# Performance work log

Measured on AMD Instinct MI355X. Metric: run time of the kernel, lower is better.

## Reference

```python
import jax, jax.numpy as jnp
import numpy as np

B, S, H = 2, 4096, 2048
NH, NKV, HD = 16, 4, 128          # heads, kv heads, head_dim = H // NH
GS_RATIO = 0.25                    # hardcoded in MyAttention.forward
ROPE_BASE = 10000.0


def rotate_half(x):
    h = x.shape[-1] // 2
    return jnp.concatenate((-x[..., h:], x[..., :h]), axis=-1)


def setup_inputs() -> dict:
    key = jax.random.key(0)
    ks = jax.random.split(key, 5)
    g = int(S * GS_RATIO)
    hidden_states = jax.random.normal(ks[0], (B, S, H), jnp.float32)
    position_ids = jnp.tile(jnp.arange(S, dtype=jnp.int32)[None, :], (B, 1))
    # causal additive mask per group window (0 keep, -1e9 masked)
    i = jnp.arange(g)
    causal = i[None, :] <= i[:, None]
    attention_mask = jnp.broadcast_to(
        jnp.where(causal, 0.0, -1e9).astype(jnp.float32)[None, None], (B, 1, g, g)
    )
    sc = 0.02
    Wq = (jax.random.normal(ks[1], (H, NH * HD), jnp.float32) * sc)
    Wk = (jax.random.normal(ks[2], (H, NKV * HD), jnp.float32) * sc)
    Wv = (jax.random.normal(ks[3], (H, NKV * HD), jnp.float32) * sc)
    Wo = (jax.random.normal(ks[4], (NH * HD, H), jnp.float32) * sc)
    return {"hidden_states": hidden_states, "attention_mask": attention_mask,
            "position_ids": position_ids, "Wq": Wq, "Wk": Wk, "Wv": Wv, "Wo": Wo}


def reference(hidden_states, attention_mask, position_ids, Wq, Wk, Wv, Wo):
    B_, S_, H_ = hidden_states.shape
    g = int(S_ * GS_RATIO)
    ng = S_ // g
    n_rep = NH // NKV

    # QKV projections -> (B, heads, S, HD)
    q = (hidden_states @ Wq).reshape(B_, S_, NH, HD).transpose(0, 2, 1, 3)
    k = (hidden_states @ Wk).reshape(B_, S_, NKV, HD).transpose(0, 2, 1, 3)
    v = (hidden_states @ Wv).reshape(B_, S_, NKV, HD).transpose(0, 2, 1, 3)

    # RoPE
    inv_freq = 1.0 / (ROPE_BASE ** (jnp.arange(0, HD, 2, dtype=jnp.float32) / HD))
    t = jnp.arange(S_, dtype=jnp.float32)
    emb = jnp.concatenate([jnp.outer(t, inv_freq)] * 2, axis=-1)  # (S, HD)
    cos = jnp.cos(emb)[position_ids][:, None]  # (B,1,S,HD)
    sin = jnp.sin(emb)[position_ids][:, None]
    q = q * cos + rotate_half(q) * sin
    k = k * cos + rotate_half(k) * sin

    # GQA repeat_kv
    k = jnp.repeat(k, n_rep, axis=1)
    v = jnp.repeat(v, n_rep, axis=1)

    # S2-Attn shift: roll second half of heads by -g/2 along seq, then group
    def shift(x):
        x = jnp.concatenate([x[:, :NH // 2],
                             jnp.roll(x[:, NH // 2:], -g // 2, axis=2)], axis=1)
        return x.transpose(0, 2, 1, 3).reshape(B_ * ng, g, NH, HD).transpose(0, 2, 1, 3)

    q, k, v = shift(q), shift(k), shift(v)

    attn = jnp.einsum('bhqd,bhkd->bhqk', q, k) / np.float32(np.sqrt(HD))
    mask = jnp.tile(attention_mask, (ng, 1, 1, 1))  # (B*ng,1,g,g)
    attn = attn + mask
    attn = jax.nn.softmax(attn.astype(jnp.float32), axis=-1).astype(q.dtype)

    out = jnp.einsum('bhqk,bhkd->bhqd', attn, v)  # (B*ng, NH, g, HD)
    out = out.transpose(0, 2, 1, 3).reshape(B_, S_, NH, HD)
    # undo shift for second half of heads (+g/2 along seq)
    out = jnp.concatenate([out[:, :, :NH // 2],
                           jnp.roll(out[:, :, NH // 2:], g // 2, axis=1)], axis=2)
    out = out.reshape(B_, S_, NH * HD) @ Wo
    return out
```

## Files before the change

### kernel.cpp

```cpp
#include <hip/hip_runtime.h>
#include <math.h>

typedef unsigned short u16;
typedef short bf16x8 __attribute__((ext_vector_type(8)));
typedef float f32x4 __attribute__((ext_vector_type(4)));


__device__ __forceinline__ u16 f2bf(float x) {
  union { float f; unsigned u; } c; c.f = x;
  unsigned r = (c.u + 0x7FFFu + ((c.u >> 16) & 1u)) >> 16;
  return (u16)r;
}
__device__ __forceinline__ float bf2f(u16 x) {
  union { unsigned u; float f; } c; c.u = ((unsigned)x) << 16;
  return c.f;
}

#define GLD16(gp, lp)                                                   \
  __builtin_amdgcn_global_load_lds(                                     \
      (__attribute__((address_space(1))) void*)(gp),                    \
      (__attribute__((address_space(3))) void*)(lp), 16, 0, 0)

__global__ __launch_bounds__(256) void cast_bf16_vec(
    const float* __restrict__ X, u16* __restrict__ Y) {
  const size_t i = ((size_t)blockIdx.x * 256 + threadIdx.x) * 4;
  float4 v = *(const float4*)(X + i);
  ushort4 o;
  o.x = f2bf(v.x); o.y = f2bf(v.y); o.z = f2bf(v.z); o.w = f2bf(v.w);
  *(ushort4*)(Y + i) = o;
}

__global__ __launch_bounds__(256) void wt_cast(
    const float* __restrict__ W, u16* __restrict__ Wt, int K, int N) {
  const int bk = blockIdx.y * 64;
  const int bn = blockIdx.x * 64;
  __shared__ float T[64 * 65];
  const int tid = threadIdx.x;
  #pragma unroll
  for (int u = 0; u < 16; ++u) {
    int idx = tid + u * 256;
    int kl = idx >> 6, nl = idx & 63;
    T[kl * 65 + nl] = W[(size_t)(bk + kl) * N + bn + nl];
  }
  __syncthreads();
  #pragma unroll
  for (int u = 0; u < 16; ++u) {
    int idx = tid + u * 256;
    int nl = idx >> 6, kl = idx & 63;
    Wt[(size_t)(bn + nl) * K + bk + kl] = f2bf(T[kl * 65 + nl]);
  }
}

__global__ __launch_bounds__(256) void gemm_bf16(
    const u16* __restrict__ A, const u16* __restrict__ Bt,
    float* __restrict__ Cf, u16* __restrict__ Cb, int M, int N, int K) {
  __shared__ u16 As[128 * 32];
  __shared__ u16 Bs[128 * 32];

  const int tid = threadIdx.x;
  const int bm = blockIdx.y * 128;
  const int bn = blockIdx.x * 128;
  const int w = tid >> 6, lane = tid & 63;
  const int col = lane & 15, quad = lane >> 4;
  const int mblk = (w & 1) * 64, nblk = (w >> 1) * 64;

  const int srow = tid >> 2;
  const int sseg = (tid & 3) * 8;

  const u16* ag0 = A + (size_t)(bm + srow) * K + sseg;
  const u16* ag1 = A + (size_t)(bm + 64 + srow) * K + sseg;
  const u16* bg0 = Bt + (size_t)(bn + srow) * K + sseg;
  const u16* bg1 = Bt + (size_t)(bn + 64 + srow) * K + sseg;
  u16* al = &As[srow * 32 + sseg];
  u16* bl = &Bs[srow * 32 + sseg];

  f32x4 acc[4][4];
  #pragma unroll
  for (int i = 0; i < 4; ++i)
    #pragma unroll
    for (int j = 0; j < 4; ++j) acc[i][j] = (f32x4)(0.0f);

  for (int k0 = 0; k0 < K; k0 += 32) {
    __syncthreads();
    GLD16(ag0 + k0, al);
    GLD16(ag1 + k0, al + 64 * 32);
    GLD16(bg0 + k0, bl);
    GLD16(bg1 + k0, bl + 64 * 32);
    __syncthreads();

    bf16x8 af[4], bfr[4];
    #pragma unroll
    for (int i = 0; i < 4; ++i)
      af[i] = *(const bf16x8*)&As[(mblk + 16 * i + col) * 32 + quad * 8];
    #pragma unroll
    for (int j = 0; j < 4; ++j)
      bfr[j] = *(const bf16x8*)&Bs[(nblk + 16 * j + col) * 32 + quad * 8];
    #pragma unroll
    for (int i = 0; i < 4; ++i)
      #pragma unroll
      for (int j = 0; j < 4; ++j)
        acc[i][j] = __builtin_amdgcn_mfma_f32_16x16x32_bf16(af[i], bfr[j], acc[i][j], 0, 0, 0);
  }

  #pragma unroll
  for (int i = 0; i < 4; ++i) {
    const int row0 = bm + mblk + 16 * i + quad * 4;
    #pragma unroll
    for (int j = 0; j < 4; ++j) {
      const int cc = bn + nblk + 16 * j + col;
      #pragma unroll
      for (int r = 0; r < 4; ++r) {
        if (Cb) Cb[(size_t)(row0 + r) * N + cc] = f2bf(acc[i][j][r]);
        else    Cf[(size_t)(row0 + r) * N + cc] = acc[i][j][r];
      }
    }
  }
}

__global__ __launch_bounds__(256) void rope_qkv(
    u16* __restrict__ QKV, const int* __restrict__ pos) {
  const unsigned idx = blockIdx.x * 256 + threadIdx.x;
  const int d = idx & 63;
  const unsigned rest = idx >> 6;
  const int hh = rest % 20;
  const unsigned bs = rest / 20;

  const int colbase = (hh < 16) ? hh * 128 : 2048 + (hh - 16) * 128;
  u16* p = QKV + (size_t)bs * 3072 + colbase + d;
  const float x0 = bf2f(p[0]);
  const float x1 = bf2f(p[64]);
  const float t = (float)pos[bs];
  const float inv_freq = __expf((float)d * -0.14391156509676332f);
  float s, c;
  __sincosf(t * inv_freq, &s, &c);
  const float sc = (hh < 16) ? 0.08838834764831845f : 1.0f;
  p[0]  = f2bf((x0 * c - x1 * s) * sc);
  p[64] = f2bf((x1 * c + x0 * s) * sc);
}

__global__ __launch_bounds__(256) void v_transpose(
    const u16* __restrict__ QKV, u16* __restrict__ Vt) {
  const int bid = blockIdx.x;
  const int st = bid & 63;
  const int kvh = (bid >> 6) & 3;
  const int b = bid >> 8;
  __shared__ u16 T[64 * 136];
  const int tid = threadIdx.x;
  #pragma unroll
  for (int u = 0; u < 4; ++u) {
    int idx = tid + u * 256;
    int sl = idx >> 4, ch = idx & 15;
    *(uint4*)&T[sl * 136 + ch * 8] =
        *(const uint4*)(QKV + ((size_t)(b * 4096 + st * 64 + sl)) * 3072 + 2560 + kvh * 128 + ch * 8);
  }
  __syncthreads();
  #pragma unroll
  for (int u = 0; u < 32; ++u) {
    int idx = tid + u * 256;
    int d = idx >> 6, sl = idx & 63;
    Vt[((size_t)((b * 4 + kvh) * 128 + d)) * 4096 + st * 64 + sl] = T[sl * 136 + d];
  }
}

__global__ __launch_bounds__(256) void attn_mfma(
    const u16* __restrict__ QKV, const u16* __restrict__ Vt,
    u16* __restrict__ Ob) {
  __shared__ u16 Ks[64 * 136];
  __shared__ u16 Vs[128 * 72];
  __shared__ u16 Ps[4][16 * 72];

  const int bid = blockIdx.x;
  const int qt = 15 - (bid & 15);
  const int h  = (bid >> 4) & 15;
  const int gi = (bid >> 8) & 3;
  const int b  = bid >> 10;

  const int tid = threadIdx.x;
  const int w = tid >> 6, lane = tid & 63;
  const int col = lane & 15, quad = lane >> 4;

  const int shift = (h >= 8) ? 512 : 0;
  const int base_s = gi * 1024;
  const int kvh = h >> 2;

  const int sq0 = (base_s + qt * 64 + shift) & 4095;
  {
    const u16* qsrc = QKV + ((size_t)(b * 4096 + sq0)) * 3072 + h * 128;
    #pragma unroll
    for (int u = 0; u < 4; ++u) {
      int idx = tid + u * 256;
      int row = idx >> 4, ch = idx & 15;
      *(uint4*)&Ks[row * 136 + ch * 8] =
          *(const uint4*)(qsrc + (size_t)row * 3072 + ch * 8);
    }
  }
  __syncthreads();
  bf16x8 aq[4];
  #pragma unroll
  for (int kk = 0; kk < 4; ++kk)
    aq[kk] = *(const bf16x8*)&Ks[(w * 16 + col) * 136 + kk * 32 + quad * 8];

  f32x4 o[8];
  #pragma unroll
  for (int jd = 0; jd < 8; ++jd) o[jd] = (f32x4)(0.0f);
  float lp[4] = {0.0f, 0.0f, 0.0f, 0.0f};

  u16* Pw = &Ps[w][0];
  const int qrow_l = w * 16 + quad * 4;

  for (int kt = 0; kt <= qt; ++kt) {
    const int sk0 = (base_s + kt * 64 + shift) & 4095;
    __syncthreads();
    {
      const u16* ksrc = QKV + ((size_t)(b * 4096 + sk0)) * 3072 + 2048 + kvh * 128;
      #pragma unroll
      for (int u = 0; u < 4; ++u) {
        int idx = tid + u * 256;
        int row = idx >> 4, ch = idx & 15;
        *(uint4*)&Ks[row * 136 + ch * 8] =
            *(const uint4*)(ksrc + (size_t)row * 3072 + ch * 8);
      }
      const u16* vsrc = Vt + ((size_t)((b * 4 + kvh) * 128)) * 4096 + sk0;
      #pragma unroll
      for (int u = 0; u < 4; ++u) {
        int idx = tid + u * 256;
        int d = idx >> 3, ch = idx & 7;
        *(uint4*)&Vs[d * 72 + ch * 8] =
            *(const uint4*)(vsrc + (size_t)d * 4096 + ch * 8);
      }
    }
    __syncthreads();

    f32x4 sc[4];
    #pragma unroll
    for (int j = 0; j < 4; ++j) sc[j] = (f32x4)(0.0f);
    #pragma unroll
    for (int kk = 0; kk < 4; ++kk) {
      #pragma unroll
      for (int j = 0; j < 4; ++j) {
        bf16x8 bk = *(const bf16x8*)&Ks[(16 * j + col) * 136 + kk * 32 + quad * 8];
        sc[j] = __builtin_amdgcn_mfma_f32_16x16x32_bf16(aq[kk], bk, sc[j], 0, 0, 0);
      }
    }

    #pragma unroll
    for (int j = 0; j < 4; ++j) {
      #pragma unroll
      for (int r = 0; r < 4; ++r) {
        float p = __expf(sc[j][r]);
        if (kt == qt && (16 * j + col) > (qrow_l + r)) p = 0.0f;
        lp[r] += p;
        Pw[(quad * 4 + r) * 72 + 16 * j + col] = f2bf(p);
      }
    }

    #pragma unroll
    for (int ks = 0; ks < 2; ++ks) {
      bf16x8 ap = *(const bf16x8*)&Pw[col * 72 + ks * 32 + quad * 8];
      #pragma unroll
      for (int jd = 0; jd < 8; ++jd) {
        bf16x8 bv = *(const bf16x8*)&Vs[(16 * jd + col) * 72 + ks * 32 + quad * 8];
        o[jd] = __builtin_amdgcn_mfma_f32_16x16x32_bf16(ap, bv, o[jd], 0, 0, 0);
      }
    }
  }

  #pragma unroll
  for (int r = 0; r < 4; ++r) {
    lp[r] += __shfl_xor(lp[r], 1, 64);
    lp[r] += __shfl_xor(lp[r], 2, 64);
    lp[r] += __shfl_xor(lp[r], 4, 64);
    lp[r] += __shfl_xor(lp[r], 8, 64);
  }

  #pragma unroll
  for (int r = 0; r < 4; ++r) {
    const int qg = qt * 64 + w * 16 + quad * 4 + r;
    const int sq = (base_s + qg + shift) & 4095;
    u16* dst = Ob + ((size_t)(b * 4096 + sq)) * 2048 + h * 128;
    const float inv = 1.0f / lp[r];
    #pragma unroll
    for (int jd = 0; jd < 8; ++jd)
      dst[16 * jd + col] = f2bf(o[jd][r] * inv);
  }
}

extern "C" void kernel_launch(void* const* d_in, const int* in_sizes, int n_in,
                              void* d_out, int out_size, void* d_ws, size_t ws_size,
                              hipStream_t stream) {
  const float* hs = (const float*)d_in[0];
  const int*   pos = (const int*)d_in[2];
  const float* Wq = (const float*)d_in[3];
  const float* Wk = (const float*)d_in[4];
  const float* Wv = (const float*)d_in[5];
  const float* Wo = (const float*)d_in[6];

  char* ws = (char*)d_ws;
  u16* hsb   = (u16*)ws; ws += (size_t)8192 * 2048 * 2;
  u16* Wqkvt = (u16*)ws; ws += (size_t)3072 * 2048 * 2;
  u16* Wot   = (u16*)ws; ws += (size_t)2048 * 2048 * 2;
  u16* QKVb  = (u16*)ws; ws += (size_t)8192 * 3072 * 2;
  u16* Vtt   = (u16*)ws; ws += (size_t)2 * 4 * 128 * 4096 * 2;
  u16* Obh   = (u16*)ws; ws += (size_t)8192 * 2048 * 2;

  dim3 blk(256);

  cast_bf16_vec<<<16384, blk, 0, stream>>>(hs, hsb);
  wt_cast<<<dim3(32, 32), blk, 0, stream>>>(Wq, Wqkvt, 2048, 2048);
  wt_cast<<<dim3(8, 32),  blk, 0, stream>>>(Wk, Wqkvt + (size_t)2048 * 2048, 2048, 512);
  wt_cast<<<dim3(8, 32),  blk, 0, stream>>>(Wv, Wqkvt + (size_t)2560 * 2048, 2048, 512);
  wt_cast<<<dim3(32, 32), blk, 0, stream>>>(Wo, Wot, 2048, 2048);

  gemm_bf16<<<dim3(24, 64), blk, 0, stream>>>(hsb, Wqkvt, nullptr, QKVb, 8192, 3072, 2048);

  rope_qkv<<<40960, blk, 0, stream>>>(QKVb, pos);

  v_transpose<<<512, blk, 0, stream>>>(QKVb, Vtt);

  attn_mfma<<<2048, blk, 0, stream>>>(QKVb, Vtt, Obh);

  gemm_bf16<<<dim3(16, 64), blk, 0, stream>>>(Obh, Wot, (float*)d_out, nullptr, 8192, 2048, 2048);
}
```

Measured before the change: 584.5 us.

## Replace GEMM with 256x256-tile, 512-thread, multi-buffered pipelined kernel

Both projection GEMMs move to a new kernel with 256x256 output tiles and 8 waves. It uses a 4-deep LDS ring with prefetch two k-steps ahead via global_load_lds, plus an XOR swizzle against LDS bank conflicts. Workgroup IDs are remapped so consecutive tiles land on the same XCD for L2 reuse, and s_setprio and split MFMA phases interleave loads with compute. The aim is to raise data reuse and hide memory latency, at the cost of a larger LDS footprint (64KB) and fewer, larger workgroups.

```diff
diff --git a/kernel.cpp b/kernel.cpp
--- a/kernel.cpp
+++ b/kernel.cpp
@@ -51,63 +51,120 @@
   }
 }
 
-__global__ __launch_bounds__(256) void gemm_bf16(
+__global__ __launch_bounds__(512) void gemm_bf16_256(
     const u16* __restrict__ A, const u16* __restrict__ Bt,
     float* __restrict__ Cf, u16* __restrict__ Cb, int M, int N, int K) {
-  __shared__ u16 As[128 * 32];
-  __shared__ u16 Bs[128 * 32];
+  __shared__ u16 As[4][256 * 32];
+  __shared__ u16 Bs[4][256 * 32];
 
   const int tid = threadIdx.x;
-  const int bm = blockIdx.y * 128;
-  const int bn = blockIdx.x * 128;
+
+  const int gridN = N >> 8;
+  const int nwg = gridDim.x * gridDim.y;
+  const int orig = blockIdx.y * gridDim.x + blockIdx.x;
+  const int q8 = nwg >> 3, r8 = nwg & 7;
+  const int xcd = orig & 7, lid = orig >> 3;
+  const int wgid = (xcd < r8 ? xcd * (q8 + 1) : r8 * (q8 + 1) + (xcd - r8) * q8) + lid;
+  const int bm = (wgid / gridN) << 8;
+  const int bn = (wgid % gridN) << 8;
+
   const int w = tid >> 6, lane = tid & 63;
   const int col = lane & 15, quad = lane >> 4;
-  const int mblk = (w & 1) * 64, nblk = (w >> 1) * 64;
+  const int wm = w >> 2, wn = w & 3;
+  const int sw = (col >> 1) & 3;
 
   const int srow = tid >> 2;
-  const int sseg = (tid & 3) * 8;
-
-  const u16* ag0 = A + (size_t)(bm + srow) * K + sseg;
-  const u16* ag1 = A + (size_t)(bm + 64 + srow) * K + sseg;
-  const u16* bg0 = Bt + (size_t)(bn + srow) * K + sseg;
-  const u16* bg1 = Bt + (size_t)(bn + 64 + srow) * K + sseg;
-  u16* al = &As[srow * 32 + sseg];
-  u16* bl = &Bs[srow * 32 + sseg];
-
-  f32x4 acc[4][4];
-  #pragma unroll
-  for (int i = 0; i < 4; ++i)
+  const int scp  = tid & 3;
+  const int sc   = scp ^ ((srow >> 1) & 3);
+
+  const u16* Ag = A  + (size_t)bm * K;
+  const u16* Bg = Bt + (size_t)bn * K;
+  const u16* aS0 = Ag + (size_t)srow * K + sc * 8;
+  const u16* aS1 = Ag + (size_t)(srow + 128) * K + sc * 8;
+  const u16* bS0 = Bg + (size_t)srow * K + sc * 8;
+  const u16* bS1 = Bg + (size_t)(srow + 128) * K + sc * 8;
+  const int ldst0 = srow * 32 + scp * 8;
+  const int ldst1 = (srow + 128) * 32 + scp * 8;
+
+#define STAGE_A(t, buf) { GLD16(aS0 + (size_t)(t) * 32, &As[buf][ldst0]); \
+                          GLD16(aS1 + (size_t)(t) * 32, &As[buf][ldst1]); }
+#define STAGE_B(t, buf) { GLD16(bS0 + (size_t)(t) * 32, &Bs[buf][ldst0]); \
+                          GLD16(bS1 + (size_t)(t) * 32, &Bs[buf][ldst1]); }
+
+  f32x4 acc[8][4];
+  #pragma unroll
+  for (int i = 0; i < 8; ++i)
     #pragma unroll
     for (int j = 0; j < 4; ++j) acc[i][j] = (f32x4)(0.0f);
 
-  for (int k0 = 0; k0 < K; k0 += 32) {
-    __syncthreads();
-    GLD16(ag0 + k0, al);
-    GLD16(ag1 + k0, al + 64 * 32);
-    GLD16(bg0 + k0, bl);
-    GLD16(bg1 + k0, bl + 64 * 32);
-    __syncthreads();
+  const int NT = K >> 5;
+
+  STAGE_A(0, 0); STAGE_B(0, 0);
+  if (NT > 1) {
+    STAGE_A(1, 1); STAGE_B(1, 1);
+    asm volatile("s_waitcnt vmcnt(4)" ::: "memory");
+  } else {
+    asm volatile("s_waitcnt vmcnt(0)" ::: "memory");
+  }
+  __builtin_amdgcn_s_barrier();
+  asm volatile("" ::: "memory");
+
+  const int aoff = (wm * 128 + col) * 32 + (quad ^ sw) * 8;
+  const int boff = (wn * 64  + col) * 32 + (quad ^ sw) * 8;
+
+  for (int t = 0; t < NT; ++t) {
+    const int cur = t & 3;
+    const bool pf = (t + 2 < NT);
+    const int pbuf = (t + 2) & 3;
 
     bf16x8 af[4], bfr[4];
     #pragma unroll
     for (int i = 0; i < 4; ++i)
-      af[i] = *(const bf16x8*)&As[(mblk + 16 * i + col) * 32 + quad * 8];
+      af[i] = *(const bf16x8*)&As[cur][aoff + (16 * i) * 32];
     #pragma unroll
     for (int j = 0; j < 4; ++j)
-      bfr[j] = *(const bf16x8*)&Bs[(nblk + 16 * j + col) * 32 + quad * 8];
+      bfr[j] = *(const bf16x8*)&Bs[cur][boff + (16 * j) * 32];
+    if (pf) STAGE_A(t + 2, pbuf);
+    __builtin_amdgcn_s_barrier();
+    asm volatile("s_waitcnt lgkmcnt(0)");
+    __builtin_amdgcn_s_setprio(1);
     #pragma unroll
     for (int i = 0; i < 4; ++i)
       #pragma unroll
       for (int j = 0; j < 4; ++j)
         acc[i][j] = __builtin_amdgcn_mfma_f32_16x16x32_bf16(af[i], bfr[j], acc[i][j], 0, 0, 0);
-  }
-
-  #pragma unroll
-  for (int i = 0; i < 4; ++i) {
-    const int row0 = bm + mblk + 16 * i + quad * 4;
+    __builtin_amdgcn_s_setprio(0);
+    __builtin_amdgcn_s_barrier();
+
+    bf16x8 af2[4];
+    #pragma unroll
+    for (int i = 0; i < 4; ++i)
+      af2[i] = *(const bf16x8*)&As[cur][aoff + ((64 + 16 * i)) * 32];
+    if (pf) STAGE_B(t + 2, pbuf);
+    __builtin_amdgcn_s_barrier();
+    asm volatile("s_waitcnt lgkmcnt(0)");
+    __builtin_amdgcn_s_setprio(1);
+    #pragma unroll
+    for (int i = 0; i < 4; ++i)
+      #pragma unroll
+      for (int j = 0; j < 4; ++j)
+        acc[4 + i][j] = __builtin_amdgcn_mfma_f32_16x16x32_bf16(af2[i], bfr[j], acc[4 + i][j], 0, 0, 0);
+    __builtin_amdgcn_s_setprio(0);
+
+    if (pf) asm volatile("s_waitcnt vmcnt(4)" ::: "memory");
+    else    asm volatile("s_waitcnt vmcnt(0)" ::: "memory");
+    __builtin_amdgcn_s_barrier();
+    asm volatile("" ::: "memory");
+  }
+
+  const int crow0 = bm + wm * 128 + quad * 4;
+  const int ccol0 = bn + wn * 64 + col;
+  #pragma unroll
+  for (int i = 0; i < 8; ++i) {
+    const int row0 = crow0 + 16 * i;
     #pragma unroll
     for (int j = 0; j < 4; ++j) {
-      const int cc = bn + nblk + 16 * j + col;
+      const int cc = ccol0 + 16 * j;
       #pragma unroll
       for (int r = 0; r < 4; ++r) {
         if (Cb) Cb[(size_t)(row0 + r) * N + cc] = f2bf(acc[i][j][r]);
@@ -115,6 +172,8 @@
       }
     }
   }
+#undef STAGE_A
+#undef STAGE_B
 }
 
 __global__ __launch_bounds__(256) void rope_qkv(
@@ -311,7 +370,7 @@
   wt_cast<<<dim3(8, 32),  blk, 0, stream>>>(Wv, Wqkvt + (size_t)2560 * 2048, 2048, 512);
   wt_cast<<<dim3(32, 32), blk, 0, stream>>>(Wo, Wot, 2048, 2048);
 
-  gemm_bf16<<<dim3(24, 64), blk, 0, stream>>>(hsb, Wqkvt, nullptr, QKVb, 8192, 3072, 2048);
+  gemm_bf16_256<<<dim3(12, 32), dim3(512), 0, stream>>>(hsb, Wqkvt, nullptr, QKVb, 8192, 3072, 2048);
 
   rope_qkv<<<40960, blk, 0, stream>>>(QKVb, pos);
 
@@ -319,5 +378,5 @@
 
   attn_mfma<<<2048, blk, 0, stream>>>(QKVb, Vtt, Obh);
 
-  gemm_bf16<<<dim3(16, 64), blk, 0, stream>>>(Obh, Wot, (float*)d_out, nullptr, 8192, 2048, 2048);
-}
+  gemm_bf16_256<<<dim3(8, 32), dim3(512), 0, stream>>>(Obh, Wot, (float*)d_out, nullptr, 8192, 2048, 2048);
+}
```

New measurement: 517.2 us. -11.5%, faster.
